# Performance work log

Measured on AMD Instinct MI355X. Metric: run time of the kernel, lower is better.

Reference implementation:

```python
import jax, jax.numpy as jnp
import numpy as np

EPS = 1.1920929e-07  # torch nn.RMSNorm default eps = finfo(fp32).eps
H, NOPE, ROPE, VD = 16, 128, 64, 128
QKD = NOPE + ROPE


def rmsnorm(x, w):
    return x * jax.lax.rsqrt(jnp.mean(x * x, axis=-1, keepdims=True) + EPS) * w


def rope(x, cos, sin):
    # x: [B,S,h,D]; cos/sin broadcast to [B,S,h,D//2]; pairs are (even, odd) interleaved
    x2 = x.reshape(*x.shape[:-1], -1, 2)
    x0, x1 = x2[..., 0], x2[..., 1]
    r = x0 * cos - x1 * sin
    i = x0 * sin + x1 * cos
    return jnp.stack([r, i], axis=-1).reshape(x.shape)


def setup_inputs() -> dict:
    key = jax.random.key(0)
    ks = jax.random.split(key, 8)
    B, S, D = 2, 2048, 2048
    QR, KR = 1536, 512
    x = jax.random.normal(ks[0], (B, S, D), jnp.float32)
    # RoPE table: theta=10000, rope dim 64 -> 32 frequencies
    pos = np.arange(S)[:, None]
    inv = 1.0 / (10000.0 ** (np.arange(0, ROPE, 2) / ROPE))[None, :]
    ang = pos * inv
    freqs_cos = jnp.asarray(np.cos(ang), jnp.float32)
    freqs_sin = jnp.asarray(np.sin(ang), jnp.float32)

    def w(k, out_dim, in_dim):
        return jax.random.normal(k, (out_dim, in_dim), jnp.float32) / np.sqrt(in_dim)

    return {
        "x": x,
        "freqs_cos": freqs_cos,
        "freqs_sin": freqs_sin,
        "Wq_down": w(ks[1], QR, D),
        "q_norm_w": jnp.ones((QR,), jnp.float32),
        "Wq_up": w(ks[2], H * QKD, QR),
        "Wkv_down": w(ks[3], ROPE + KR, D),
        "kv_norm_w": jnp.ones((KR,), jnp.float32),
        "Wkv_up": w(ks[4], H * (VD + NOPE), KR),
        "Wo": w(ks[5], D, H * VD),
        "bo": jnp.zeros((D,), jnp.float32),
        "start_pos": 0,
    }


def reference(x, freqs_cos, freqs_sin, Wq_down, q_norm_w, Wq_up, Wkv_down, kv_norm_w, Wkv_up, Wo, bo, start_pos):
    B, S, D = x.shape
    cos = freqs_cos[None, :, None, :]
    sin = freqs_sin[None, :, None, :]
    # low-rank Q path: down -> RMSNorm -> up
    q = rmsnorm(x @ Wq_down.T, q_norm_w) @ Wq_up.T
    q = q.reshape(B, S, H, QKD)
    q_nope, q_rope = q[..., :NOPE], q[..., NOPE:]
    q_rope = rope(q_rope, cos, sin)
    q = jnp.concatenate([q_nope, q_rope], axis=-1)  # [B,S,H,QKD]
    # low-rank KV path: shared rope part + latent kv
    kv = x @ Wkv_down.T
    k_rope, c_kv = kv[..., :ROPE], kv[..., ROPE:]
    k_rope = rope(k_rope[:, :, None, :], cos, sin)  # [B,S,1,ROPE]
    kv = rmsnorm(c_kv, kv_norm_w) @ Wkv_up.T
    kv = kv.reshape(B, S, H, NOPE + VD)
    k_nope, v = kv[..., :NOPE], kv[..., NOPE:]
    k = jnp.concatenate([k_nope, jnp.broadcast_to(k_rope, (B, S, H, ROPE))], axis=-1)
    # causal SDPA (start_pos=0 prefill: cache slice equals fresh K/V)
    scale = 1.0 / np.sqrt(QKD)
    scores = jnp.einsum("bqhd,bkhd->bhqk", q, k) * scale
    mask = jnp.tril(jnp.ones((S, S), bool))
    scores = jnp.where(mask, scores, -jnp.inf)
    attn = jax.nn.softmax(scores, axis=-1)
    o = jnp.einsum("bhqk,bkhd->bqhd", attn, v).reshape(B, S, H * VD)
    return o @ Wo.T + bo
```

## Files before the change

kernel.cpp:

```cpp
#include <hip/hip_runtime.h>
#include <stdint.h>


typedef short bf16x8 __attribute__((ext_vector_type(8)));
typedef float f32x4  __attribute__((ext_vector_type(4)));
typedef unsigned int u32;

#define RMS_EPS 1.1920929e-07f
#define SCALE_L2E 0.10411931095f

__device__ __forceinline__ unsigned short f2b(float f) {
  union { float f; uint32_t u; } c; c.f = f;
  uint32_t u = c.u;
  return (unsigned short)((u + 0x7FFFu + ((u >> 16) & 1u)) >> 16);
}
__device__ __forceinline__ float b2f(short s) {
  union { uint32_t u; float f; } c; c.u = ((uint32_t)(unsigned short)s) << 16;
  return c.f;
}
__device__ __forceinline__ void gld16(const short* g, short* l) {
  __builtin_amdgcn_global_load_lds(
      (const __attribute__((address_space(1))) u32*)g,
      (__attribute__((address_space(3))) u32*)l, 16, 0, 0);
}

__global__ void f2bf_kernel(const float* __restrict__ in, short* __restrict__ out, int n4) {
  int i = blockIdx.x * 256 + threadIdx.x;
  if (i >= n4) return;
  float4 v = ((const float4*)in)[i];
  union { ushort4 s; uint2 u; } o;
  o.s.x = f2b(v.x); o.s.y = f2b(v.y); o.s.z = f2b(v.z); o.s.w = f2b(v.w);
  ((uint2*)out)[i] = o.u;
}

__global__ void f2bf_pad_kernel(const float* __restrict__ in, short* __restrict__ out,
                                int n4, int cols4, int src_rows) {
  int i = blockIdx.x * 256 + threadIdx.x;
  if (i >= n4) return;
  int row = i / cols4;
  ushort4 s = {0, 0, 0, 0};
  if (row < src_rows) {
    float4 v = ((const float4*)in)[i];
    s.x = f2b(v.x); s.y = f2b(v.y); s.z = f2b(v.z); s.w = f2b(v.w);
  }
  union { ushort4 ss; uint2 u; } o; o.ss = s;
  ((uint2*)out)[i] = o.u;
}

template <int EPI>
__global__ __launch_bounds__(256) void gemm_bt(
    const short* __restrict__ A, const short* __restrict__ Bt,
    void* __restrict__ Cv, const float* __restrict__ bias,
    int K, int ldc,
    const float* __restrict__ fc, const float* __restrict__ fs,
    short* __restrict__ aux) {
  __shared__ __align__(16) short As[128 * 32];
  __shared__ __align__(16) short Bs[128 * 32];
  int row0 = blockIdx.y * 128, col0 = blockIdx.x * 128;
  int t = threadIdx.x, lane = t & 63, w = t >> 6;
  int wm = w >> 1, wn = w & 1;
  int l15 = lane & 15, l4 = lane >> 4;
  f32x4 acc[4][4] = {};

  int srow = lane >> 2, scol = (lane & 3) * 8;
  const short* Ag = A + (size_t)(row0 + srow) * K + scol;
  const short* Bg = Bt + (size_t)(col0 + srow) * K + scol;

  for (int kt = 0; kt < K; kt += 32) {
#pragma unroll
    for (int c = 0; c < 2; ++c) {
      int blk = w * 2 + c;
      gld16(Ag + (size_t)(blk * 16) * K + kt, As + blk * 512);
      gld16(Bg + (size_t)(blk * 16) * K + kt, Bs + blk * 512);
    }
    __syncthreads();
    bf16x8 af[4], bfr[4];
#pragma unroll
    for (int i = 0; i < 4; ++i) {
      af[i]  = *(const bf16x8*)(As + (wm * 64 + i * 16 + l15) * 32 + l4 * 8);
      bfr[i] = *(const bf16x8*)(Bs + (wn * 64 + i * 16 + l15) * 32 + l4 * 8);
    }
#pragma unroll
    for (int i = 0; i < 4; ++i)
#pragma unroll
      for (int j = 0; j < 4; ++j)
        acc[i][j] = __builtin_amdgcn_mfma_f32_16x16x32_bf16(af[i], bfr[j], acc[i][j], 0, 0, 0);
    __syncthreads();
  }

  if constexpr (EPI == 0) {
    float* C = (float*)Cv;
#pragma unroll
    for (int j = 0; j < 4; ++j) {
      int col = col0 + wn * 64 + j * 16 + l15;
      float bv = bias ? bias[col] : 0.0f;
#pragma unroll
      for (int i = 0; i < 4; ++i) {
        int row = row0 + wm * 64 + i * 16 + l4 * 4;
        float* dst = C + (size_t)row * ldc + col;
#pragma unroll
        for (int r = 0; r < 4; ++r) dst[(size_t)r * ldc] = acc[i][j][r] + bv;
      }
    }
  } else if constexpr (EPI == 1) {
    short* C = (short*)Cv;
#pragma unroll
    for (int j = 0; j < 4; ++j) {
      int col = col0 + wn * 64 + j * 16 + l15;
#pragma unroll
      for (int i = 0; i < 4; ++i) {
        int row = row0 + wm * 64 + i * 16 + l4 * 4;
        short* dst = C + (size_t)row * ldc + col;
#pragma unroll
        for (int r = 0; r < 4; ++r) dst[(size_t)r * ldc] = (short)f2b(acc[i][j][r]);
      }
    }
  } else if constexpr (EPI == 2) {
    short* qb = (short*)Cv;
#pragma unroll
    for (int j = 0; j < 4; ++j) {
      int col = col0 + wn * 64 + j * 16 + l15;
      int h = col / 192;
      int d = col - h * 192;
      bool ro = (d >= 128);
      int ir = ro ? ((d - 128) >> 1) : 0;
      bool odd = (l15 & 1);
#pragma unroll
      for (int i = 0; i < 4; ++i) {
        int rowb = row0 + wm * 64 + i * 16 + l4 * 4;
#pragma unroll
        for (int r = 0; r < 4; ++r) {
          int row = rowb + r;
          int b = row >> 11, s = row & 2047;
          float v = acc[i][j][r];
          float pv = __shfl_xor(v, 1);
          float o;
          if (ro) {
            float c = fc[s * 32 + ir], sn = fs[s * 32 + ir];
            o = odd ? (pv * sn + v * c) : (v * c - pv * sn);
          } else {
            o = v;
          }
          qb[((size_t)((b * 16 + h) * 2048 + s)) * 192 + d] = (short)f2b(o * SCALE_L2E);
        }
      }
    }
  } else {
    short* kb = (short*)Cv;
    short* vT = aux;
    int h = col0 >> 8;
    if ((col0 & 128) == 0) {
#pragma unroll
      for (int j = 0; j < 4; ++j) {
        int d = wn * 64 + j * 16 + l15;
#pragma unroll
        for (int i = 0; i < 4; ++i) {
          int rowb = row0 + wm * 64 + i * 16 + l4 * 4;
#pragma unroll
          for (int r = 0; r < 4; ++r) {
            int row = rowb + r;
            int b = row >> 11, s = row & 2047;
            kb[((size_t)((b * 16 + h) * 2048 + s)) * 192 + d] = (short)f2b(acc[i][j][r]);
          }
        }
      }
    } else {
#pragma unroll
      for (int j = 0; j < 4; ++j) {
        int dv = wn * 64 + j * 16 + l15;
#pragma unroll
        for (int i = 0; i < 4; ++i) {
          int s0 = row0 + wm * 64 + i * 16 + l4 * 4;
          int b = s0 >> 11, s = s0 & 2047;
          short4 o;
          o.x = (short)f2b(acc[i][j][0]);
          o.y = (short)f2b(acc[i][j][1]);
          o.z = (short)f2b(acc[i][j][2]);
          o.w = (short)f2b(acc[i][j][3]);
          *(short4*)(vT + ((size_t)((b * 16 + h) * 128 + dv)) * 2048 + s) = o;
        }
      }
    }
  }
}

template <int W>
__global__ __launch_bounds__(256) void rmsnorm_wave(
    const short* __restrict__ in, const float* __restrict__ wgt,
    short* __restrict__ out, int ld_in) {
  constexpr int NC = W / 512;
  int row = blockIdx.x * 4 + (threadIdx.x >> 6);
  int lane = threadIdx.x & 63;
  const short* x = in + (size_t)row * ld_in + lane * 8;
  float vals[NC * 8];
  float ss = 0.f;
#pragma unroll
  for (int c = 0; c < NC; ++c) {
    bf16x8 v = *(const bf16x8*)(x + c * 512);
#pragma unroll
    for (int k = 0; k < 8; ++k) {
      float f = b2f(v[k]);
      vals[c * 8 + k] = f; ss += f * f;
    }
  }
#pragma unroll
  for (int off = 32; off > 0; off >>= 1) ss += __shfl_xor(ss, off);
  float rs = rsqrtf(ss / (float)W + RMS_EPS);
  short* o = out + (size_t)row * W + lane * 8;
#pragma unroll
  for (int c = 0; c < NC; ++c) {
    const float4* wp = (const float4*)(wgt + c * 512 + lane * 8);
    float4 w0 = wp[0], w1 = wp[1];
    ushort4 lo, hi;
    lo.x = f2b(vals[c * 8 + 0] * rs * w0.x);
    lo.y = f2b(vals[c * 8 + 1] * rs * w0.y);
    lo.z = f2b(vals[c * 8 + 2] * rs * w0.z);
    lo.w = f2b(vals[c * 8 + 3] * rs * w0.w);
    hi.x = f2b(vals[c * 8 + 4] * rs * w1.x);
    hi.y = f2b(vals[c * 8 + 5] * rs * w1.y);
    hi.z = f2b(vals[c * 8 + 6] * rs * w1.z);
    hi.w = f2b(vals[c * 8 + 7] * rs * w1.w);
    *(ushort4*)(o + c * 512) = lo;
    *(ushort4*)(o + c * 512 + 4) = hi;
  }
}

__global__ void prep_krope_kernel(const short* __restrict__ c1,
                                  const float* __restrict__ fc,
                                  const float* __restrict__ fs,
                                  short* __restrict__ kb) {
  int idx = blockIdx.x * 256 + threadIdx.x;
  int i = idx & 31;
  int s = (idx >> 5) & 2047;
  int b = idx >> 16;
  const short* row = c1 + (size_t)(b * 2048 + s) * 2176 + 1536 + 2 * i;
  float x0 = b2f(row[0]), x1 = b2f(row[1]);
  float c = fc[s * 32 + i], sn = fs[s * 32 + i];
  uint32_t pk = (uint32_t)f2b(x0 * c - x1 * sn) | ((uint32_t)f2b(x0 * sn + x1 * c) << 16);
  size_t base = ((size_t)(b * 16) * 2048 + s) * 192 + 128 + 2 * i;
#pragma unroll
  for (int h = 0; h < 16; ++h)
    *(uint32_t*)(kb + base + (size_t)h * 2048 * 192) = pk;
}

__global__ __launch_bounds__(256) void attn_kernel(
    const short* __restrict__ qb, const short* __restrict__ kb,
    const short* __restrict__ vtb, short* __restrict__ ob) {
  __shared__ __align__(16) short Ks[64 * 200];
  __shared__ __align__(16) short Vs[128 * 72];
  __shared__ __align__(16) short Ps[4][16 * 72];
  int bid = blockIdx.x;
  int xcd = bid & 7, kk2 = bid >> 3;
  int bh = xcd * 4 + (kk2 >> 4);
  int qx = kk2 & 15;
  int b = bh >> 4, h = bh & 15;
  int t = threadIdx.x, lane = t & 63, w = t >> 6;
  int l15 = lane & 15, l4 = lane >> 4;
  const short* Kbh = kb + (size_t)bh * 2048 * 192;
  const short* Vbh = vtb + (size_t)bh * 128 * 2048;

  for (int half = 0; half < 2; ++half) {
    int qt = half ? (31 - qx) : qx;
    int q0 = qt * 64;
    const short* Qbase = qb + ((size_t)bh * 2048 + q0 + w * 16) * 192;
    bf16x8 qf[6];
#pragma unroll
    for (int kk = 0; kk < 6; ++kk)
      qf[kk] = *(const bf16x8*)(Qbase + (size_t)l15 * 192 + kk * 32 + l4 * 8);
    f32x4 oacc[8] = {};
    float m_i[4] = {-1e30f, -1e30f, -1e30f, -1e30f};
    float l_i[4] = {0.f, 0.f, 0.f, 0.f};
    int kend = q0 + 64;

    for (int kt = 0; kt < kend; kt += 64) {
#pragma unroll
      for (int c = 0; c < 6; ++c) {
        int idx = t + 256 * c;
        int r = idx / 24, ch = idx - r * 24;
        *(bf16x8*)(Ks + r * 200 + ch * 8) =
            *(const bf16x8*)(Kbh + (size_t)(kt + r) * 192 + ch * 8);
      }
#pragma unroll
      for (int c = 0; c < 4; ++c) {
        int idx = t + 256 * c;
        int d = idx >> 3, cc = (idx & 7) * 8;
        *(bf16x8*)(Vs + d * 72 + cc) =
            *(const bf16x8*)(Vbh + (size_t)d * 2048 + kt + cc);
      }
      __syncthreads();

      f32x4 s[4] = {};
      __builtin_amdgcn_s_setprio(1);
#pragma unroll
      for (int kk = 0; kk < 6; ++kk) {
#pragma unroll
        for (int c = 0; c < 4; ++c) {
          bf16x8 kf = *(const bf16x8*)(Ks + (c * 16 + l15) * 200 + kk * 32 + l4 * 8);
          s[c] = __builtin_amdgcn_mfma_f32_16x16x32_bf16(qf[kk], kf, s[c], 0, 0, 0);
        }
      }
      __builtin_amdgcn_s_setprio(0);
      bool diag = (kt == q0);
      int qrow = q0 + w * 16 + l4 * 4;
#pragma unroll
      for (int r = 0; r < 4; ++r) {
        float sv[4];
#pragma unroll
        for (int c = 0; c < 4; ++c) {
          sv[c] = s[c][r];
          if (diag) {
            int col = kt + c * 16 + l15;
            if (col > qrow + r) sv[c] = -1e30f;
          }
        }
        float tm = fmaxf(fmaxf(sv[0], sv[1]), fmaxf(sv[2], sv[3]));
#pragma unroll
        for (int off = 1; off < 16; off <<= 1) tm = fmaxf(tm, __shfl_xor(tm, off));
        float newm = fmaxf(m_i[r], tm);
        float alpha = __builtin_amdgcn_exp2f(m_i[r] - newm);
        float rs = 0.f;
#pragma unroll
        for (int c = 0; c < 4; ++c) {
          float p = __builtin_amdgcn_exp2f(sv[c] - newm);
          sv[c] = p; rs += p;
        }
#pragma unroll
        for (int off = 1; off < 16; off <<= 1) rs += __shfl_xor(rs, off);
        l_i[r] = l_i[r] * alpha + rs;
        m_i[r] = newm;
#pragma unroll
        for (int dt = 0; dt < 8; ++dt) oacc[dt][r] *= alpha;
        short* prow = &Ps[w][(l4 * 4 + r) * 72];
#pragma unroll
        for (int c = 0; c < 4; ++c) prow[c * 16 + l15] = (short)f2b(sv[c]);
      }
      bf16x8 pf0 = *(const bf16x8*)(&Ps[w][l15 * 72 + l4 * 8]);
      bf16x8 pf1 = *(const bf16x8*)(&Ps[w][l15 * 72 + 32 + l4 * 8]);
      __builtin_amdgcn_s_setprio(1);
#pragma unroll
      for (int dt = 0; dt < 8; ++dt) {
        bf16x8 vf0 = *(const bf16x8*)(Vs + (dt * 16 + l15) * 72 + l4 * 8);
        bf16x8 vf1 = *(const bf16x8*)(Vs + (dt * 16 + l15) * 72 + 32 + l4 * 8);
        oacc[dt] = __builtin_amdgcn_mfma_f32_16x16x32_bf16(pf0, vf0, oacc[dt], 0, 0, 0);
        oacc[dt] = __builtin_amdgcn_mfma_f32_16x16x32_bf16(pf1, vf1, oacc[dt], 0, 0, 0);
      }
      __builtin_amdgcn_s_setprio(0);
      __syncthreads();
    }
#pragma unroll
    for (int r = 0; r < 4; ++r) {
      float inv = 1.0f / l_i[r];
      int row = q0 + w * 16 + l4 * 4 + r;
      short* dst = ob + ((size_t)(b * 2048 + row)) * 2048 + h * 128;
#pragma unroll
      for (int dt = 0; dt < 8; ++dt)
        dst[dt * 16 + l15] = (short)f2b(oacc[dt][r] * inv);
    }
  }
}

extern "C" void kernel_launch(void* const* d_in, const int* in_sizes, int n_in,
                              void* d_out, int out_size, void* d_ws, size_t ws_size,
                              hipStream_t stream) {
  const float* x    = (const float*)d_in[0];
  const float* fcos = (const float*)d_in[1];
  const float* fsin = (const float*)d_in[2];
  const float* Wqd  = (const float*)d_in[3];
  const float* qnw  = (const float*)d_in[4];
  const float* Wqu  = (const float*)d_in[5];
  const float* Wkvd = (const float*)d_in[6];
  const float* kvnw = (const float*)d_in[7];
  const float* Wkvu = (const float*)d_in[8];
  const float* Wo   = (const float*)d_in[9];
  const float* bo   = (const float*)d_in[10];
  float* out = (float*)d_out;
  char* ws = (char*)d_ws;

  short* x_bf  = (short*)(ws + 0);
  short* w_cat = (short*)(ws + 16777216);
  short* w_qu  = (short*)(ws + 25690112);
  short* w_kvu = (short*)(ws + 35127296);
  short* w_o   = (short*)(ws + 39321600);
  short* c1    = (short*)(ws + 47710208);
  short* qn    = (short*)(ws + 65536000);
  short* ckvn  = (short*)(ws + 78118912);
  short* q_b   = (short*)(ws + 82313216);
  short* k_b   = (short*)(ws + 107479040);
  short* vT    = (short*)(ws + 132644864);
  short* o_bf  = (short*)(ws + 149422080);

  f2bf_kernel<<<8192, 256, 0, stream>>>(x, x_bf, 2097152);
  f2bf_kernel<<<3072, 256, 0, stream>>>(Wqd, w_cat, 786432);
  f2bf_pad_kernel<<<1280, 256, 0, stream>>>(Wkvd, w_cat + 1536 * 2048, 327680, 512, 576);
  f2bf_kernel<<<4608, 256, 0, stream>>>(Wqu, w_qu, 1179648);
  f2bf_kernel<<<2048, 256, 0, stream>>>(Wkvu, w_kvu, 524288);
  f2bf_kernel<<<4096, 256, 0, stream>>>(Wo, w_o, 1048576);

  gemm_bt<1><<<dim3(17, 32), 256, 0, stream>>>(x_bf, w_cat, c1, nullptr, 2048, 2176,
                                               nullptr, nullptr, nullptr);
  prep_krope_kernel<<<512, 256, 0, stream>>>(c1, fcos, fsin, k_b);
  rmsnorm_wave<1536><<<1024, 256, 0, stream>>>(c1, qnw, qn, 2176);
  rmsnorm_wave<512><<<1024, 256, 0, stream>>>(c1 + 1600, kvnw, ckvn, 2176);

  gemm_bt<2><<<dim3(24, 32), 256, 0, stream>>>(qn, w_qu, q_b, nullptr, 1536, 0,
                                               fcos, fsin, nullptr);
  gemm_bt<3><<<dim3(32, 32), 256, 0, stream>>>(ckvn, w_kvu, k_b, nullptr, 512, 0,
                                               nullptr, nullptr, vT);

  attn_kernel<<<512, 256, 0, stream>>>(q_b, k_b, vT, o_bf);

  gemm_bt<0><<<dim3(16, 32), 256, 0, stream>>>(o_bf, w_o, out, bo, 2048, 2048,
                                               nullptr, nullptr, nullptr);
}
```

Before: 380.9 us.

## Prefetch K/V tiles into registers, add lazy softmax rescale, swizzle GEMM blocks

The attention kernel now loads the next K/V tile into registers while the current tile is computed, so global-load latency overlaps the MFMA work, and the barrier moves to the top of the loop. The online softmax only rescales the running max and accumulators when the new max exceeds the old one by more than a threshold, which skips exp2 calls and accumulator multiplies on most tiles. The GEMM remaps block indices so neighbouring blocks are spread across XCDs to improve cache locality. The costs are higher register pressure from the prefetch buffers, and a risk of reduced precision or overflow if the threshold logic lets values grow too large.

```diff
diff --git a/kernel.cpp b/kernel.cpp
--- a/kernel.cpp
+++ b/kernel.cpp
@@ -56,7 +56,11 @@
     short* __restrict__ aux) {
   __shared__ __align__(16) short As[128 * 32];
   __shared__ __align__(16) short Bs[128 * 32];
-  int row0 = blockIdx.y * 128, col0 = blockIdx.x * 128;
+  int nx = gridDim.x;
+  int lin = blockIdx.y * nx + blockIdx.x;
+  int cpx = (nx * gridDim.y) >> 3;
+  int swz = (lin & 7) * cpx + (lin >> 3);
+  int row0 = (swz / nx) * 128, col0 = (swz % nx) * 128;
   int t = threadIdx.x, lane = t & 63, w = t >> 6;
   int wm = w >> 1, wn = w & 1;
   int l15 = lane & 15, l4 = lane >> 4;
@@ -259,6 +263,18 @@
   const short* Kbh = kb + (size_t)bh * 2048 * 192;
   const short* Vbh = vtb + (size_t)bh * 128 * 2048;
 
+  int sk_r[6], sk_c[6], sv_d[4], sv_c[4];
+#pragma unroll
+  for (int c = 0; c < 6; ++c) {
+    int idx = t + 256 * c;
+    sk_r[c] = idx / 24; sk_c[c] = (idx - sk_r[c] * 24) * 8;
+  }
+#pragma unroll
+  for (int c = 0; c < 4; ++c) {
+    int idx = t + 256 * c;
+    sv_d[c] = idx >> 3; sv_c[c] = (idx & 7) * 8;
+  }
+
   for (int half = 0; half < 2; ++half) {
     int qt = half ? (31 - qx) : qx;
     int q0 = qt * 64;
@@ -272,20 +288,29 @@
     float l_i[4] = {0.f, 0.f, 0.f, 0.f};
     int kend = q0 + 64;
 
+    bf16x8 kr[6], vr[4];
+#pragma unroll
+    for (int c = 0; c < 6; ++c)
+      kr[c] = *(const bf16x8*)(Kbh + (size_t)sk_r[c] * 192 + sk_c[c]);
+#pragma unroll
+    for (int c = 0; c < 4; ++c)
+      vr[c] = *(const bf16x8*)(Vbh + (size_t)sv_d[c] * 2048 + sv_c[c]);
+
     for (int kt = 0; kt < kend; kt += 64) {
-#pragma unroll
-      for (int c = 0; c < 6; ++c) {
-        int idx = t + 256 * c;
-        int r = idx / 24, ch = idx - r * 24;
-        *(bf16x8*)(Ks + r * 200 + ch * 8) =
-            *(const bf16x8*)(Kbh + (size_t)(kt + r) * 192 + ch * 8);
-      }
-#pragma unroll
-      for (int c = 0; c < 4; ++c) {
-        int idx = t + 256 * c;
-        int d = idx >> 3, cc = (idx & 7) * 8;
-        *(bf16x8*)(Vs + d * 72 + cc) =
-            *(const bf16x8*)(Vbh + (size_t)d * 2048 + kt + cc);
+      __syncthreads();
+#pragma unroll
+      for (int c = 0; c < 6; ++c)
+        *(bf16x8*)(Ks + sk_r[c] * 200 + sk_c[c]) = kr[c];
+#pragma unroll
+      for (int c = 0; c < 4; ++c)
+        *(bf16x8*)(Vs + sv_d[c] * 72 + sv_c[c]) = vr[c];
+      if (kt + 64 < kend) {
+#pragma unroll
+        for (int c = 0; c < 6; ++c)
+          kr[c] = *(const bf16x8*)(Kbh + (size_t)(kt + 64 + sk_r[c]) * 192 + sk_c[c]);
+#pragma unroll
+        for (int c = 0; c < 4; ++c)
+          vr[c] = *(const bf16x8*)(Vbh + (size_t)sv_d[c] * 2048 + kt + 64 + sv_c[c]);
       }
       __syncthreads();
 
@@ -316,20 +341,23 @@
         float tm = fmaxf(fmaxf(sv[0], sv[1]), fmaxf(sv[2], sv[3]));
 #pragma unroll
         for (int off = 1; off < 16; off <<= 1) tm = fmaxf(tm, __shfl_xor(tm, off));
-        float newm = fmaxf(m_i[r], tm);
-        float alpha = __builtin_amdgcn_exp2f(m_i[r] - newm);
+        if (__any(tm - m_i[r] > 6.0f)) {
+          float newm = fmaxf(m_i[r], tm);
+          float alpha = __builtin_amdgcn_exp2f(m_i[r] - newm);
+          m_i[r] = newm;
+          l_i[r] *= alpha;
+#pragma unroll
+          for (int dt = 0; dt < 8; ++dt) oacc[dt][r] *= alpha;
+        }
         float rs = 0.f;
 #pragma unroll
         for (int c = 0; c < 4; ++c) {
-          float p = __builtin_amdgcn_exp2f(sv[c] - newm);
+          float p = __builtin_amdgcn_exp2f(sv[c] - m_i[r]);
           sv[c] = p; rs += p;
         }
 #pragma unroll
         for (int off = 1; off < 16; off <<= 1) rs += __shfl_xor(rs, off);
-        l_i[r] = l_i[r] * alpha + rs;
-        m_i[r] = newm;
-#pragma unroll
-        for (int dt = 0; dt < 8; ++dt) oacc[dt][r] *= alpha;
+        l_i[r] += rs;
         short* prow = &Ps[w][(l4 * 4 + r) * 72];
 #pragma unroll
         for (int c = 0; c < 4; ++c) prow[c * 16 + l15] = (short)f2b(sv[c]);
@@ -345,7 +373,6 @@
         oacc[dt] = __builtin_amdgcn_mfma_f32_16x16x32_bf16(pf1, vf1, oacc[dt], 0, 0, 0);
       }
       __builtin_amdgcn_s_setprio(0);
-      __syncthreads();
     }
 #pragma unroll
     for (int r = 0; r < 4; ++r) {
```

Result: slower. 487.1 us (+27.9%).

## Transpose attention MFMA so softmax is per-lane and P moves via bpermute

Applied to the files above, without the earlier changes.

The attention kernel now computes S^T (K as the A operand, Q as B), so each lane owns a single query column. The online-softmax max and sum need only two cross-lane shuffles, and m/l become scalars. The probabilities are packed to bf16 pairs and redistributed with ds_bpermute instead of a round trip through shared memory, and the output is written as packed 8-byte stores. Separately, the GEMM remaps its block index across 8 groups (one per XCD) to improve L2 locality. The trade-off is extra bpermute and select instructions plus more intricate lane-index logic.

```diff
diff --git a/kernel.cpp b/kernel.cpp
--- a/kernel.cpp
+++ b/kernel.cpp
@@ -1,4 +1,5 @@
 #include <hip/hip_runtime.h>
+#include <hip/hip_bf16.h>
 #include <stdint.h>
 
 
@@ -17,6 +18,11 @@
 __device__ __forceinline__ float b2f(short s) {
   union { uint32_t u; float f; } c; c.u = ((uint32_t)(unsigned short)s) << 16;
   return c.f;
+}
+__device__ __forceinline__ u32 pk2(float a, float b) {
+  union { __hip_bfloat162 h; u32 u; } cv;
+  cv.h = __float22bfloat162_rn(float2{a, b});
+  return cv.u;
 }
 __device__ __forceinline__ void gld16(const short* g, short* l) {
   __builtin_amdgcn_global_load_lds(
@@ -56,7 +62,11 @@
     short* __restrict__ aux) {
   __shared__ __align__(16) short As[128 * 32];
   __shared__ __align__(16) short Bs[128 * 32];
-  int row0 = blockIdx.y * 128, col0 = blockIdx.x * 128;
+  int nx = gridDim.x;
+  int lin = blockIdx.y * nx + blockIdx.x;
+  int cpx = (nx * gridDim.y) >> 3;
+  int swz = (lin & 7) * cpx + (lin >> 3);
+  int row0 = (swz / nx) * 128, col0 = (swz % nx) * 128;
   int t = threadIdx.x, lane = t & 63, w = t >> 6;
   int wm = w >> 1, wn = w & 1;
   int l15 = lane & 15, l4 = lane >> 4;
@@ -248,7 +258,6 @@
     const short* __restrict__ vtb, short* __restrict__ ob) {
   __shared__ __align__(16) short Ks[64 * 200];
   __shared__ __align__(16) short Vs[128 * 72];
-  __shared__ __align__(16) short Ps[4][16 * 72];
   int bid = blockIdx.x;
   int xcd = bid & 7, kk2 = bid >> 3;
   int bh = xcd * 4 + (kk2 >> 4);
@@ -259,6 +268,10 @@
   const short* Kbh = kb + (size_t)bh * 2048 * 192;
   const short* Vbh = vtb + (size_t)bh * 128 * 2048;
 
+  int sA = (l15 + ((l4 & 1) << 5)) << 2;
+  int sB = sA + (16 << 2);
+  bool chi = (l4 >> 1) != 0;
+
   for (int half = 0; half < 2; ++half) {
     int qt = half ? (31 - qx) : qx;
     int q0 = qt * 64;
@@ -267,9 +280,9 @@
 #pragma unroll
     for (int kk = 0; kk < 6; ++kk)
       qf[kk] = *(const bf16x8*)(Qbase + (size_t)l15 * 192 + kk * 32 + l4 * 8);
-    f32x4 oacc[8] = {};
-    float m_i[4] = {-1e30f, -1e30f, -1e30f, -1e30f};
-    float l_i[4] = {0.f, 0.f, 0.f, 0.f};
+    f32x4 oaccT[8] = {};
+    float m_i = -1e30f, l_i = 0.f;
+    int qcol = q0 + w * 16 + l15;
     int kend = q0 + 64;
 
     for (int kt = 0; kt < kend; kt += 64) {
@@ -296,65 +309,94 @@
 #pragma unroll
         for (int c = 0; c < 4; ++c) {
           bf16x8 kf = *(const bf16x8*)(Ks + (c * 16 + l15) * 200 + kk * 32 + l4 * 8);
-          s[c] = __builtin_amdgcn_mfma_f32_16x16x32_bf16(qf[kk], kf, s[c], 0, 0, 0);
+          s[c] = __builtin_amdgcn_mfma_f32_16x16x32_bf16(kf, qf[kk], s[c], 0, 0, 0);
         }
       }
       __builtin_amdgcn_s_setprio(0);
-      bool diag = (kt == q0);
-      int qrow = q0 + w * 16 + l4 * 4;
-#pragma unroll
-      for (int r = 0; r < 4; ++r) {
-        float sv[4];
-#pragma unroll
-        for (int c = 0; c < 4; ++c) {
-          sv[c] = s[c][r];
-          if (diag) {
-            int col = kt + c * 16 + l15;
-            if (col > qrow + r) sv[c] = -1e30f;
+
+      if (kt == q0) {
+#pragma unroll
+        for (int c = 0; c < 4; ++c)
+#pragma unroll
+          for (int r = 0; r < 4; ++r) {
+            int k = kt + c * 16 + l4 * 4 + r;
+            if (k > qcol) s[c][r] = -1e30f;
           }
+      }
+      float mx = fmaxf(fmaxf(fmaxf(s[0][0], s[0][1]), fmaxf(s[0][2], s[0][3])),
+                       fmaxf(fmaxf(s[1][0], s[1][1]), fmaxf(s[1][2], s[1][3])));
+      mx = fmaxf(mx, fmaxf(fmaxf(fmaxf(s[2][0], s[2][1]), fmaxf(s[2][2], s[2][3])),
+                           fmaxf(fmaxf(s[3][0], s[3][1]), fmaxf(s[3][2], s[3][3]))));
+      mx = fmaxf(mx, __shfl_xor(mx, 16));
+      mx = fmaxf(mx, __shfl_xor(mx, 32));
+      float newm = fmaxf(m_i, mx);
+      float alpha = __builtin_amdgcn_exp2f(m_i - newm);
+      float rs = 0.f;
+#pragma unroll
+      for (int c = 0; c < 4; ++c)
+#pragma unroll
+        for (int r = 0; r < 4; ++r) {
+          float p = __builtin_amdgcn_exp2f(s[c][r] - newm);
+          s[c][r] = p; rs += p;
         }
-        float tm = fmaxf(fmaxf(sv[0], sv[1]), fmaxf(sv[2], sv[3]));
-#pragma unroll
-        for (int off = 1; off < 16; off <<= 1) tm = fmaxf(tm, __shfl_xor(tm, off));
-        float newm = fmaxf(m_i[r], tm);
-        float alpha = __builtin_amdgcn_exp2f(m_i[r] - newm);
-        float rs = 0.f;
-#pragma unroll
-        for (int c = 0; c < 4; ++c) {
-          float p = __builtin_amdgcn_exp2f(sv[c] - newm);
-          sv[c] = p; rs += p;
-        }
-#pragma unroll
-        for (int off = 1; off < 16; off <<= 1) rs += __shfl_xor(rs, off);
-        l_i[r] = l_i[r] * alpha + rs;
-        m_i[r] = newm;
-#pragma unroll
-        for (int dt = 0; dt < 8; ++dt) oacc[dt][r] *= alpha;
-        short* prow = &Ps[w][(l4 * 4 + r) * 72];
-#pragma unroll
-        for (int c = 0; c < 4; ++c) prow[c * 16 + l15] = (short)f2b(sv[c]);
-      }
-      bf16x8 pf0 = *(const bf16x8*)(&Ps[w][l15 * 72 + l4 * 8]);
-      bf16x8 pf1 = *(const bf16x8*)(&Ps[w][l15 * 72 + 32 + l4 * 8]);
+      rs += __shfl_xor(rs, 16);
+      rs += __shfl_xor(rs, 32);
+      l_i = l_i * alpha + rs;
+      m_i = newm;
+#pragma unroll
+      for (int dt = 0; dt < 8; ++dt)
+#pragma unroll
+        for (int r = 0; r < 4; ++r) oaccT[dt][r] *= alpha;
+
+      u32 pk00 = pk2(s[0][0], s[0][1]), pk01 = pk2(s[0][2], s[0][3]);
+      u32 pk10 = pk2(s[1][0], s[1][1]), pk11 = pk2(s[1][2], s[1][3]);
+      u32 pk20 = pk2(s[2][0], s[2][1]), pk21 = pk2(s[2][2], s[2][3]);
+      u32 pk30 = pk2(s[3][0], s[3][1]), pk31 = pk2(s[3][2], s[3][3]);
+      union { bf16x8 v; u32 u[4]; } P0, P1;
+      {
+        u32 a0 = __builtin_amdgcn_ds_bpermute(sA, (int)pk00);
+        u32 a1 = __builtin_amdgcn_ds_bpermute(sA, (int)pk01);
+        u32 a2 = __builtin_amdgcn_ds_bpermute(sB, (int)pk00);
+        u32 a3 = __builtin_amdgcn_ds_bpermute(sB, (int)pk01);
+        u32 b0 = __builtin_amdgcn_ds_bpermute(sA, (int)pk10);
+        u32 b1 = __builtin_amdgcn_ds_bpermute(sA, (int)pk11);
+        u32 b2 = __builtin_amdgcn_ds_bpermute(sB, (int)pk10);
+        u32 b3 = __builtin_amdgcn_ds_bpermute(sB, (int)pk11);
+        P0.u[0] = chi ? b0 : a0; P0.u[1] = chi ? b1 : a1;
+        P0.u[2] = chi ? b2 : a2; P0.u[3] = chi ? b3 : a3;
+      }
+      {
+        u32 a0 = __builtin_amdgcn_ds_bpermute(sA, (int)pk20);
+        u32 a1 = __builtin_amdgcn_ds_bpermute(sA, (int)pk21);
+        u32 a2 = __builtin_amdgcn_ds_bpermute(sB, (int)pk20);
+        u32 a3 = __builtin_amdgcn_ds_bpermute(sB, (int)pk21);
+        u32 b0 = __builtin_amdgcn_ds_bpermute(sA, (int)pk30);
+        u32 b1 = __builtin_amdgcn_ds_bpermute(sA, (int)pk31);
+        u32 b2 = __builtin_amdgcn_ds_bpermute(sB, (int)pk30);
+        u32 b3 = __builtin_amdgcn_ds_bpermute(sB, (int)pk31);
+        P1.u[0] = chi ? b0 : a0; P1.u[1] = chi ? b1 : a1;
+        P1.u[2] = chi ? b2 : a2; P1.u[3] = chi ? b3 : a3;
+      }
+
       __builtin_amdgcn_s_setprio(1);
 #pragma unroll
       for (int dt = 0; dt < 8; ++dt) {
         bf16x8 vf0 = *(const bf16x8*)(Vs + (dt * 16 + l15) * 72 + l4 * 8);
         bf16x8 vf1 = *(const bf16x8*)(Vs + (dt * 16 + l15) * 72 + 32 + l4 * 8);
-        oacc[dt] = __builtin_amdgcn_mfma_f32_16x16x32_bf16(pf0, vf0, oacc[dt], 0, 0, 0);
-        oacc[dt] = __builtin_amdgcn_mfma_f32_16x16x32_bf16(pf1, vf1, oacc[dt], 0, 0, 0);
+        oaccT[dt] = __builtin_amdgcn_mfma_f32_16x16x32_bf16(vf0, P0.v, oaccT[dt], 0, 0, 0);
+        oaccT[dt] = __builtin_amdgcn_mfma_f32_16x16x32_bf16(vf1, P1.v, oaccT[dt], 0, 0, 0);
       }
       __builtin_amdgcn_s_setprio(0);
       __syncthreads();
     }
-#pragma unroll
-    for (int r = 0; r < 4; ++r) {
-      float inv = 1.0f / l_i[r];
-      int row = q0 + w * 16 + l4 * 4 + r;
-      short* dst = ob + ((size_t)(b * 2048 + row)) * 2048 + h * 128;
-#pragma unroll
-      for (int dt = 0; dt < 8; ++dt)
-        dst[dt * 16 + l15] = (short)f2b(oacc[dt][r] * inv);
+    float inv = 1.0f / l_i;
+    short* dst = ob + ((size_t)(b * 2048 + qcol)) * 2048 + h * 128;
+#pragma unroll
+    for (int dt = 0; dt < 8; ++dt) {
+      uint2 o;
+      o.x = pk2(oaccT[dt][0] * inv, oaccT[dt][1] * inv);
+      o.y = pk2(oaccT[dt][2] * inv, oaccT[dt][3] * inv);
+      *(uint2*)(dst + dt * 16 + l4 * 4) = o;
     }
   }
 }
```

New measurement: 357.9 us. -6.0%, faster.
